# Kernel optimization log

Measured on AMD Instinct MI355X. Metric: run time of the kernel, lower is better.

The kernel has to match this reference:

```python
import jax, jax.numpy as jnp
import numpy as np

CTX = 2048
D_IN = 2048
D_OUT = 2048
N_HEADS = 16
HEAD_DIM = D_OUT // N_HEADS
ROPE_BASE = 10000.0


def rope_tables(head_dim, ctx):
    inv_freq = 1.0 / (ROPE_BASE ** (jnp.arange(0, head_dim, 2, dtype=jnp.float32) / head_dim))
    angles = jnp.arange(ctx, dtype=jnp.float32)[:, None] * inv_freq[None, :]  # [ctx, hd/2]
    angles = jnp.concatenate([angles, angles], axis=1)  # [ctx, hd]
    return jnp.sin(angles), jnp.cos(angles)


def apply_rope(x, sin, cos):
    # x: [b, h, s, d]; rotate-by-half (Raschka / Llama style)
    s = x.shape[2]
    d = x.shape[3]
    x1, x2 = x[..., : d // 2], x[..., d // 2 :]
    rotated = jnp.concatenate([-x2, x1], axis=-1)
    return x * cos[:s][None, None] + rotated * sin[:s][None, None]


def setup_inputs() -> dict:
    key = jax.random.key(0)
    kx, kq, kk, kv, ko = jax.random.split(key, 5)
    scale = 0.02
    return {
        "x": jax.random.normal(kx, (2, CTX, D_IN), dtype=jnp.float32),
        "W_query": jax.random.normal(kq, (D_IN, D_OUT), dtype=jnp.float32) * scale,
        "W_key": jax.random.normal(kk, (D_IN, D_OUT), dtype=jnp.float32) * scale,
        "W_value": jax.random.normal(kv, (D_IN, D_OUT), dtype=jnp.float32) * scale,
        "W_out": jax.random.normal(ko, (D_OUT, D_OUT), dtype=jnp.float32) * scale,
    }


def reference(x, W_query, W_key, W_value, W_out):
    bs, cl, _ = x.shape
    sin, cos = rope_tables(HEAD_DIM, CTX)

    def split_heads(t):  # [b, s, d_out] -> [b, h, s, hd]
        return t.reshape(bs, cl, N_HEADS, HEAD_DIM).transpose(0, 2, 1, 3)

    q = split_heads(x @ W_query)
    k = split_heads(x @ W_key)
    v = split_heads(x @ W_value)

    q = apply_rope(q, sin, cos)
    k = apply_rope(k, sin, cos)

    # NOTE: original module does NOT scale by 1/sqrt(head_dim)
    scores = jnp.einsum("bhqd,bhkd->bhqk", q, k)
    causal = jnp.triu(jnp.ones((cl, cl), dtype=bool), k=1)
    scores = jnp.where(causal[None, None], -jnp.inf, scores)
    weights = jax.nn.softmax(scores, axis=-1)
    ctx = jnp.einsum("bhqk,bhkd->bhqd", weights, v)
    ctx = ctx.transpose(0, 2, 1, 3).reshape(bs, cl, N_HEADS * HEAD_DIM)
    return ctx @ W_out
```

## Files before the change

### kernel.cpp

```cpp
#include <hip/hip_runtime.h>
#include <cstdint>
#include <cstddef>

typedef _Float16 f16;
typedef _Float16 f16x8 __attribute__((ext_vector_type(8)));
typedef _Float16 f16x4 __attribute__((ext_vector_type(4)));
typedef float    f32x4 __attribute__((ext_vector_type(4)));

#define S_CTX 2048
#define NH 16
#define DH 128

#define BAR() asm volatile("s_barrier" ::: "memory")
#define VMW(n) asm volatile("s_waitcnt vmcnt(" #n ")" ::: "memory")

__device__ __forceinline__ void gload16(const void* g, void* l) {
  __builtin_amdgcn_global_load_lds(
      (const __attribute__((address_space(1))) void*)g,
      (__attribute__((address_space(3))) void*)l, 16, 0, 0);
}

__global__ void prep(const float* __restrict__ x,
                     const float* __restrict__ w0, const float* __restrict__ w1,
                     const float* __restrict__ w2, const float* __restrict__ w3,
                     f16* __restrict__ xb,
                     f16* __restrict__ o0, f16* __restrict__ o1,
                     f16* __restrict__ o2, f16* __restrict__ o3,
                     float* __restrict__ sint, float* __restrict__ cost) {
  const int bid = blockIdx.x, tid = threadIdx.x;
  if (bid < 512) {
    int idx = bid * 256 + tid;
    int j = idx & 63, s = idx >> 6;
    float invf = __expf(-(float)(2 * j) * (1.0f / 128.0f) * 9.210340371976184f);
    float a = (float)s * invf;
    sint[idx] = sinf(a);
    cost[idx] = cosf(a);
  } else if (bid < 8704) {
    int i = ((bid - 512) * 256 + tid) * 4;
    float4 v = *(const float4*)(x + i);
    f16x4 o; o[0] = (f16)v.x; o[1] = (f16)v.y; o[2] = (f16)v.z; o[3] = (f16)v.w;
    *(f16x4*)(xb + i) = o;
  } else {
    int b2 = bid - 8704;
    int z = b2 >> 12, rem = b2 & 4095;
    int by = rem >> 6, bx = rem & 63;
    int tx = tid & 31, ty = tid >> 5;
    const float* in; f16* out;
    switch (z) {
      case 0: in = w0; out = o0; break;
      case 1: in = w1; out = o1; break;
      case 2: in = w2; out = o2; break;
      default: in = w3; out = o3; break;
    }
    __shared__ float tl[32][33];
    int xc = bx * 32 + tx, yc = by * 32 + ty;
#pragma unroll
    for (int r = 0; r < 32; r += 8)
      tl[ty + r][tx] = in[(size_t)(yc + r) * 2048 + xc];
    __syncthreads();
    int xo = by * 32 + tx, yo = bx * 32 + ty;
#pragma unroll
    for (int r = 0; r < 32; r += 8)
      out[(size_t)(yo + r) * 2048 + xo] = (f16)tl[tx][ty + r];
  }
}

__global__ __launch_bounds__(512, 1)
void gemm_qk(const f16* __restrict__ A, const f16* __restrict__ wqT,
             const f16* __restrict__ wkT,
             f16* __restrict__ qb, f16* __restrict__ kb,
             const float* __restrict__ sint, const float* __restrict__ cost) {
  extern __shared__ __align__(16) char lds[];
  const int tid = threadIdx.x, lane = tid & 63;
  const int wvi = tid >> 6, wm = wvi >> 2, wn = wvi & 3;
  const int gcol = blockIdx.x * 256;
  const int proj = gcol >> 11;
  const int col0 = gcol & 2047;
  const int row0 = blockIdx.y * 256;
  const f16* Bt = proj ? wkT : wqT;

  const int ca0 = tid, ca1 = tid + 512;
  const int ra0 = ca0 >> 2, ra1 = ca1 >> 2;
  const int sa0 = (ca0 & 3) ^ ((ra0 >> 1) & 3);
  const int sa1 = (ca1 & 3) ^ ((ra1 >> 1) & 3);
  const f16* gA0 = A + (size_t)(row0 + ra0) * 2048 + sa0 * 8;
  const f16* gA1 = A + (size_t)(row0 + ra1) * 2048 + sa1 * 8;
  const f16* gB0 = Bt + (size_t)(col0 + ra0) * 2048 + sa0 * 8;
  const f16* gB1 = Bt + (size_t)(col0 + ra1) * 2048 + sa1 * 8;

  const int kslot = lane >> 4;
  int aoff[8], boff[4];
#pragma unroll
  for (int i = 0; i < 8; i++) {
    int row = wm * 128 + i * 16 + (lane & 15);
    aoff[i] = row * 64 + ((kslot ^ ((row >> 1) & 3)) << 4);
  }
#pragma unroll
  for (int j = 0; j < 4; j++) {
    int rb = (wn >> 1) * 128 + (wn & 1) * 32 + (j & 1) * 16 + (j >> 1) * 64 + (lane & 15);
    boff[j] = rb * 64 + ((kslot ^ ((rb >> 1) & 3)) << 4);
  }

  f32x4 acc[8][4] = {};

#define QKPH(SLOT, HS, SSLOT, DOSTAGE, WN) do {                                \
    const char* As_ = lds + (SLOT) * 32768;                                    \
    const char* Bs_ = As_ + 16384;                                             \
    f16x8 af[8], bf[4];                                                        \
    _Pragma("unroll") for (int i_ = 0; i_ < 8; i_++)                           \
      af[i_] = *(const f16x8*)(As_ + aoff[i_]);                                \
    _Pragma("unroll") for (int j_ = 0; j_ < 4; j_++)                           \
      bf[j_] = *(const f16x8*)(Bs_ + boff[j_]);                                \
    if (DOSTAGE) {                                                             \
      char* dA = lds + (SSLOT) * 32768;                                        \
      gload16(gA0 + (HS) * 32, dA + ca0 * 16);                                 \
      gload16(gA1 + (HS) * 32, dA + ca1 * 16);                                 \
      gload16(gB0 + (HS) * 32, dA + 16384 + ca0 * 16);                         \
      gload16(gB1 + (HS) * 32, dA + 16384 + ca1 * 16);                         \
    }                                                                          \
    asm volatile("s_waitcnt vmcnt(" #WN ")" ::: "memory");                     \
    BAR();                                                                     \
    __builtin_amdgcn_s_setprio(1);                                             \
    _Pragma("unroll") for (int i_ = 0; i_ < 8; i_++)                           \
      _Pragma("unroll") for (int j_ = 0; j_ < 4; j_++)                         \
        acc[i_][j_] = __builtin_amdgcn_mfma_f32_16x16x32_f16(af[i_], bf[j_],   \
                                                             acc[i_][j_], 0, 0, 0); \
    __builtin_amdgcn_s_setprio(0);                                             \
    BAR();                                                                     \
  } while (0)

#pragma unroll
  for (int h = 0; h < 2; h++) {
    char* dA = lds + h * 32768;
    gload16(gA0 + h * 32, dA + ca0 * 16);
    gload16(gA1 + h * 32, dA + ca1 * 16);
    gload16(gB0 + h * 32, dA + 16384 + ca0 * 16);
    gload16(gB1 + h * 32, dA + 16384 + ca1 * 16);
  }
  VMW(4); BAR();

  for (int t = 0; t < 20; ++t) {
    const int hb = 3 * t;
    QKPH(0, hb + 2, 2, 1, 4);
    QKPH(1, hb + 3, 0, 1, 4);
    QKPH(2, hb + 4, 1, 1, 4);
  }
  QKPH(0, 62, 2, 1, 4);
  QKPH(1, 63, 0, 1, 4);
  QKPH(2, 0, 0, 0, 0);
  QKPH(0, 0, 0, 0, 63);
#undef QKPH

  const int b = row0 >> 11, sb = row0 & 2047;
  f16* dst = proj ? kb : qb;
  const int h = (col0 >> 7) + (wn >> 1);
#pragma unroll
  for (int i = 0; i < 8; i++)
#pragma unroll
    for (int jj = 0; jj < 2; jj++)
#pragma unroll
      for (int r = 0; r < 4; r++) {
        int s = sb + wm * 128 + i * 16 + (lane >> 4) * 4 + r;
        int d = (wn & 1) * 32 + jj * 16 + (lane & 15);
        float cv = cost[s * 64 + d], sv = sint[s * 64 + d];
        float x1 = acc[i][jj][r], x2 = acc[i][jj + 2][r];
        size_t base = ((size_t)(b * NH + h) * S_CTX + s) << 7;
        dst[base + d]      = (f16)(x1 * cv - x2 * sv);
        dst[base + d + 64] = (f16)(x2 * cv + x1 * sv);
      }
}

template<int MODE>
__global__ __launch_bounds__(512, 1)
void gemm8(const f16* __restrict__ A, const f16* __restrict__ Bt,
           f16* __restrict__ vtb, float* __restrict__ of) {
  extern __shared__ __align__(16) char lds[];
#define RING_A(e) (lds + (e) * 16384)
#define RING_B(e) (lds + 65536 + (e) * 8192)
  const int tid = threadIdx.x, lane = tid & 63;
  const int wvi = tid >> 6, wm = wvi >> 1, wn = wvi & 1;
  const int col0 = blockIdx.x * 128;
  const int row0 = blockIdx.y * 256;

  const int ca0 = tid, ca1 = tid + 512, cb0 = tid;
  const int rAs0 = ca0 >> 2, rAs1 = ca1 >> 2, rBs0 = cb0 >> 2;
  const int sA0 = (ca0 & 3) ^ ((rAs0 >> 1) & 3);
  const int sA1 = (ca1 & 3) ^ ((rAs1 >> 1) & 3);
  const int sB0 = (cb0 & 3) ^ ((rBs0 >> 1) & 3);
  const f16* gA0 = A + (size_t)(row0 + rAs0) * 2048 + sA0 * 8;
  const f16* gA1 = A + (size_t)(row0 + rAs1) * 2048 + sA1 * 8;
  const f16* gB0 = Bt + (size_t)(col0 + rBs0) * 2048 + sB0 * 8;

  const int kslot = lane >> 4;
  int aoff[4], boff[4];
#pragma unroll
  for (int i = 0; i < 4; i++) {
    int row = wm * 64 + i * 16 + (lane & 15);
    aoff[i] = row * 64 + ((kslot ^ ((row >> 1) & 3)) << 4);
  }
#pragma unroll
  for (int j = 0; j < 4; j++) {
    int rb = wn * 32 + (j & 1) * 16 + (j >> 1) * 64 + (lane & 15);
    boff[j] = rb * 64 + ((kslot ^ ((rb >> 1) & 3)) << 4);
  }

  f32x4 acc[4][4] = {};

#define PH8(SLOT, HS, DOSTAGE, WN) do {                                        \
    const char* As_ = RING_A(SLOT);                                            \
    const char* Bs_ = RING_B(SLOT);                                            \
    f16x8 af[4], bf[4];                                                        \
    _Pragma("unroll") for (int i_ = 0; i_ < 4; i_++)                           \
      af[i_] = *(const f16x8*)(As_ + aoff[i_]);                                \
    _Pragma("unroll") for (int j_ = 0; j_ < 4; j_++)                           \
      bf[j_] = *(const f16x8*)(Bs_ + boff[j_]);                                \
    if (DOSTAGE) {                                                             \
      gload16(gA0 + (HS) * 32, RING_A((HS) & 3) + ca0 * 16);                   \
      gload16(gA1 + (HS) * 32, RING_A((HS) & 3) + ca1 * 16);                   \
      gload16(gB0 + (HS) * 32, RING_B((HS) & 3) + cb0 * 16);                   \
    }                                                                          \
    asm volatile("s_waitcnt vmcnt(" #WN ")" ::: "memory");                     \
    BAR();                                                                     \
    __builtin_amdgcn_s_setprio(1);                                             \
    _Pragma("unroll") for (int i_ = 0; i_ < 4; i_++)                           \
      _Pragma("unroll") for (int j_ = 0; j_ < 4; j_++)                         \
        acc[i_][j_] = __builtin_amdgcn_mfma_f32_16x16x32_f16(af[i_], bf[j_],   \
                                                             acc[i_][j_], 0, 0, 0); \
    __builtin_amdgcn_s_setprio(0);                                             \
    BAR();                                                                     \
  } while (0)

#pragma unroll
  for (int h = 0; h < 3; h++) {
    gload16(gA0 + h * 32, RING_A(h) + ca0 * 16);
    gload16(gA1 + h * 32, RING_A(h) + ca1 * 16);
    gload16(gB0 + h * 32, RING_B(h) + cb0 * 16);
  }
  VMW(6); BAR();

  for (int t = 0; t < 15; ++t) {
    const int p = t * 4;
    PH8(0, p + 3, 1, 6);
    PH8(1, p + 4, 1, 6);
    PH8(2, p + 5, 1, 6);
    PH8(3, p + 6, 1, 6);
  }
  PH8(0, 63, 1, 6);
  PH8(1, 0, 0, 3);
  PH8(2, 0, 0, 0);
  PH8(3, 0, 0, 63);
#undef PH8

  const int b = row0 >> 11, sbase = row0 & 2047;

  if (MODE == 2) {
#pragma unroll
    for (int i = 0; i < 4; i++)
#pragma unroll
      for (int j = 0; j < 4; j++)
#pragma unroll
        for (int r = 0; r < 4; r++) {
          int row = row0 + wm * 64 + i * 16 + (lane >> 4) * 4 + r;
          int col = col0 + wn * 32 + (j & 1) * 16 + (j >> 1) * 64 + (lane & 15);
          of[(size_t)row * 2048 + col] = acc[i][j][r];
        }
  } else {
    const int h = col0 >> 7;
    f16x4* ldsv = (f16x4*)lds;
#pragma unroll
    for (int i = 0; i < 4; i++)
#pragma unroll
      for (int j = 0; j < 4; j++) {
        f16x4 v;
#pragma unroll
        for (int r = 0; r < 4; r++) v[r] = (f16)acc[i][j][r];
        int su = wm * 16 + i * 4 + (lane >> 4);
        int d  = wn * 32 + (j & 1) * 16 + (j >> 1) * 64 + (lane & 15);
        ldsv[d * 64 + (su ^ ((d << 1) & 63))] = v;
      }
    __syncthreads();
#pragma unroll
    for (int it = 0; it < 8; ++it) {
      int o = it * 512 + tid;
      int d = o >> 5, c = o & 31;
      int xc = (d << 1) & 63;
      f16x4 lo = ldsv[d * 64 + ((2 * c) ^ xc)];
      f16x4 hi = ldsv[d * 64 + ((2 * c + 1) ^ xc)];
      f16x8 vv;
      vv[0] = lo[0]; vv[1] = lo[1]; vv[2] = lo[2]; vv[3] = lo[3];
      vv[4] = hi[0]; vv[5] = hi[1]; vv[6] = hi[2]; vv[7] = hi[3];
      *(f16x8*)&vtb[((size_t)(b * NH + h) * DH + d) * S_CTX + sbase + c * 8] = vv;
    }
  }
#undef RING_A
#undef RING_B
}

__global__ __launch_bounds__(512)
void attn_k(const f16* __restrict__ q, const f16* __restrict__ kk,
            const f16* __restrict__ vt, f16* __restrict__ ctx) {
  __shared__ __align__(16) f16 Ks[2][64 * 128];
  __shared__ __align__(16) f16 Vs[2][128 * 64];
  __shared__ __align__(16) f16 Pl[8][16 * 64];
  const int tid = threadIdx.x, lane = tid & 63, wv = tid >> 6;
  const int bh = blockIdx.y;
  const int b = bh >> 4, h = bh & 15;
  const size_t plane = (size_t)bh * (S_CTX * DH);
  const f16* Qp = q + plane;
  const f16* Kp = kk + plane;
  const f16* Vp = vt + plane;
  const float LOG2E = 1.4426950408889634f;

  const int ck0 = tid, ck1 = tid + 512;
  const int cv0 = tid, cv1 = tid + 512;

  for (int half = 0; half < 2; half++) {
    const int Q = half ? (15 - (int)blockIdx.x) : (int)blockIdx.x;
    const int q0 = Q * 128;
    const int NT = 2 * Q + 2;

    f16x8 qf[4];
    {
      const f16* qq = Qp + (size_t)(q0 + wv * 16 + (lane & 15)) * DH + ((lane >> 4) * 8);
#pragma unroll
      for (int ks = 0; ks < 4; ks++) {
        qf[ks] = *(const f16x8*)(qq + ks * 32);
#pragma unroll
        for (int e = 0; e < 8; e++) qf[ks][e] = (f16)((float)qf[ks][e] * LOG2E);
      }
    }
    float m_[4], l_[4];
    f32x4 o[8] = {};
#pragma unroll
    for (int r = 0; r < 4; r++) { m_[r] = -3e38f; l_[r] = 0.f; }

    {
      int rk0 = ck0 >> 4, rk1 = ck1 >> 4;
      gload16(Kp + (size_t)rk0 * DH + (((ck0 & 15) ^ (rk0 & 7)) * 8), &Ks[0][ck0 * 8]);
      gload16(Kp + (size_t)rk1 * DH + (((ck1 & 15) ^ (rk1 & 7)) * 8), &Ks[0][ck1 * 8]);
      int rv0 = cv0 >> 3, rv1 = cv1 >> 3;
      gload16(Vp + (size_t)rv0 * S_CTX + (((cv0 & 7) ^ (rv0 & 7)) * 8), &Vs[0][cv0 * 8]);
      gload16(Vp + (size_t)rv1 * S_CTX + (((cv1 & 7) ^ (rv1 & 7)) * 8), &Vs[0][cv1 * 8]);
    }
    VMW(0); BAR();

    int cur = 0;
    for (int t = 0; t < NT; t++) {
      if (t + 1 < NT) {
        const f16* Kt = Kp + (size_t)(t + 1) * 64 * DH;
        const f16* Vt = Vp + (size_t)(t + 1) * 64;
        int nb = cur ^ 1;
        int rk0 = ck0 >> 4, rk1 = ck1 >> 4;
        gload16(Kt + (size_t)rk0 * DH + (((ck0 & 15) ^ (rk0 & 7)) * 8), &Ks[nb][ck0 * 8]);
        gload16(Kt + (size_t)rk1 * DH + (((ck1 & 15) ^ (rk1 & 7)) * 8), &Ks[nb][ck1 * 8]);
        int rv0 = cv0 >> 3, rv1 = cv1 >> 3;
        gload16(Vt + (size_t)rv0 * S_CTX + (((cv0 & 7) ^ (rv0 & 7)) * 8), &Vs[nb][cv0 * 8]);
        gload16(Vt + (size_t)rv1 * S_CTX + (((cv1 & 7) ^ (rv1 & 7)) * 8), &Vs[nb][cv1 * 8]);
      }

      const f16* Ksc = Ks[cur];
      const f16* Vsc = Vs[cur];

      f32x4 st[4] = {};
#pragma unroll
      for (int n = 0; n < 4; n++) {
        int rK = n * 16 + (lane & 15);
#pragma unroll
        for (int ks = 0; ks < 4; ks++) {
          int slot = ks * 4 + (lane >> 4);
          f16x8 kf = *(const f16x8*)&Ksc[rK * 128 + ((slot ^ (rK & 7)) << 3)];
          st[n] = __builtin_amdgcn_mfma_f32_16x16x32_f16(qf[ks], kf, st[n], 0, 0, 0);
        }
      }
      if (t >= 2 * Q) {
#pragma unroll
        for (int n = 0; n < 4; n++)
#pragma unroll
          for (int r = 0; r < 4; r++) {
            int kvc = t * 64 + n * 16 + (lane & 15);
            int qr = q0 + wv * 16 + (lane >> 4) * 4 + r;
            if (kvc > qr) st[n][r] = -3e38f;
          }
      }
      float mx[4];
#pragma unroll
      for (int r = 0; r < 4; r++)
        mx[r] = fmaxf(fmaxf(st[0][r], st[1][r]), fmaxf(st[2][r], st[3][r]));
#pragma unroll
      for (int msk = 1; msk < 16; msk <<= 1)
#pragma unroll
        for (int r = 0; r < 4; r++) mx[r] = fmaxf(mx[r], __shfl_xor(mx[r], msk));
      bool need = false;
#pragma unroll
      for (int r = 0; r < 4; r++) need = need || (mx[r] > m_[r] + 8.0f);
      if (__any(need)) {
#pragma unroll
        for (int r = 0; r < 4; r++) {
          float nm = fmaxf(m_[r], mx[r]);
          float al = __builtin_amdgcn_exp2f(m_[r] - nm);
          m_[r] = nm;
          l_[r] *= al;
#pragma unroll
          for (int j = 0; j < 8; j++) o[j][r] *= al;
        }
      }
      float ps[4] = {0.f, 0.f, 0.f, 0.f};
      float pvv[4][4];
#pragma unroll
      for (int n = 0; n < 4; n++)
#pragma unroll
        for (int r = 0; r < 4; r++) {
          float p = __builtin_amdgcn_exp2f(st[n][r] - m_[r]);
          pvv[n][r] = p; ps[r] += p;
        }
#pragma unroll
      for (int msk = 1; msk < 16; msk <<= 1)
#pragma unroll
        for (int r = 0; r < 4; r++) ps[r] += __shfl_xor(ps[r], msk);
#pragma unroll
      for (int r = 0; r < 4; r++) l_[r] += ps[r];

      f16* Pw = Pl[wv];
#pragma unroll
      for (int n = 0; n < 4; n++)
#pragma unroll
        for (int r = 0; r < 4; r++) {
          int rowp = (lane >> 4) * 4 + r;
          int colp = n * 16 + (lane & 15);
          Pw[rowp * 64 + (((colp >> 3) ^ (rowp & 7)) << 3) + (colp & 7)] = (f16)pvv[n][r];
        }
#pragma unroll
      for (int ks = 0; ks < 2; ks++) {
        int rowp = lane & 15;
        int slotp = ks * 4 + (lane >> 4);
        f16x8 pa = *(const f16x8*)&Pw[rowp * 64 + ((slotp ^ (rowp & 7)) << 3)];
#pragma unroll
        for (int j = 0; j < 8; j++) {
          int rv = j * 16 + (lane & 15);
          int slotv = ks * 4 + (lane >> 4);
          f16x8 vf = *(const f16x8*)&Vsc[rv * 64 + ((slotv ^ (rv & 7)) << 3)];
          o[j] = __builtin_amdgcn_mfma_f32_16x16x32_f16(pa, vf, o[j], 0, 0, 0);
        }
      }

      VMW(0); BAR();
      cur ^= 1;
    }

#pragma unroll
    for (int j = 0; j < 8; j++)
#pragma unroll
      for (int r = 0; r < 4; r++) {
        int qr = q0 + wv * 16 + (lane >> 4) * 4 + r;
        int dd = h * 128 + j * 16 + (lane & 15);
        ctx[((size_t)(b * S_CTX + qr) * 2048) + dd] = (f16)(o[j][r] / l_[r]);
      }
  }
}

extern "C" void kernel_launch(void* const* d_in, const int* in_sizes, int n_in,
                              void* d_out, int out_size, void* d_ws, size_t ws_size,
                              hipStream_t stream) {
  (void)in_sizes; (void)n_in; (void)out_size; (void)ws_size;
  const float* x  = (const float*)d_in[0];
  const float* Wq = (const float*)d_in[1];
  const float* Wk = (const float*)d_in[2];
  const float* Wv = (const float*)d_in[3];
  const float* Wo = (const float*)d_in[4];
  float* out = (float*)d_out;
  char* ws = (char*)d_ws;

  f16*   xb   = (f16*)(ws);
  f16*   ctxb = (f16*)(ws);
  f16*   wqT  = (f16*)(ws + 16777216);
  f16*   wkT  = (f16*)(ws + 25165824);
  f16*   wvT  = (f16*)(ws + 33554432);
  f16*   woT  = (f16*)(ws + 41943040);
  f16*   qb   = (f16*)(ws + 50331648);
  f16*   kb   = (f16*)(ws + 67108864);
  f16*   vtb  = (f16*)(ws + 83886080);
  float* sint = (float*)(ws + 100663296);
  float* cost = (float*)(ws + 101187584);

  prep<<<dim3(25088), dim3(256), 0, stream>>>(x, Wq, Wk, Wv, Wo, xb,
                                              wqT, wkT, wvT, woT, sint, cost);
  gemm_qk<<<dim3(16, 16), dim3(512), 98304, stream>>>(xb, wqT, wkT, qb, kb, sint, cost);
  gemm8<1><<<dim3(16, 16), dim3(512), 98304, stream>>>(xb, wvT, vtb, nullptr);
  attn_k<<<dim3(8, 32), dim3(512), 0, stream>>>(qb, kb, vtb, ctxb);
  gemm8<2><<<dim3(16, 16), dim3(512), 98304, stream>>>(ctxb, woT, nullptr, out);
}
```

Measured before the change: 274.9 us.

## Give each attention wave two 16-row query tiles with half the threads

```diff
diff --git a/kernel.cpp b/kernel.cpp
--- a/kernel.cpp
+++ b/kernel.cpp
@@ -13,6 +13,7 @@
 
 #define BAR() asm volatile("s_barrier" ::: "memory")
 #define VMW(n) asm volatile("s_waitcnt vmcnt(" #n ")" ::: "memory")
+#define MF(a, b, c) __builtin_amdgcn_mfma_f32_16x16x32_f16((a), (b), (c), 0, 0, 0)
 
 __device__ __forceinline__ void gload16(const void* g, void* l) {
   __builtin_amdgcn_global_load_lds(
@@ -123,8 +124,7 @@
     __builtin_amdgcn_s_setprio(1);                                             \
     _Pragma("unroll") for (int i_ = 0; i_ < 8; i_++)                           \
       _Pragma("unroll") for (int j_ = 0; j_ < 4; j_++)                         \
-        acc[i_][j_] = __builtin_amdgcn_mfma_f32_16x16x32_f16(af[i_], bf[j_],   \
-                                                             acc[i_][j_], 0, 0, 0); \
+        acc[i_][j_] = MF(af[i_], bf[j_], acc[i_][j_]);                         \
     __builtin_amdgcn_s_setprio(0);                                             \
     BAR();                                                                     \
   } while (0)
@@ -224,8 +224,7 @@
     __builtin_amdgcn_s_setprio(1);                                             \
     _Pragma("unroll") for (int i_ = 0; i_ < 4; i_++)                           \
       _Pragma("unroll") for (int j_ = 0; j_ < 4; j_++)                         \
-        acc[i_][j_] = __builtin_amdgcn_mfma_f32_16x16x32_f16(af[i_], bf[j_],   \
-                                                             acc[i_][j_], 0, 0, 0); \
+        acc[i_][j_] = MF(af[i_], bf[j_], acc[i_][j_]);                         \
     __builtin_amdgcn_s_setprio(0);                                             \
     BAR();                                                                     \
   } while (0)
@@ -296,12 +295,12 @@
 #undef RING_B
 }
 
-__global__ __launch_bounds__(512)
+__global__ __launch_bounds__(256)
 void attn_k(const f16* __restrict__ q, const f16* __restrict__ kk,
             const f16* __restrict__ vt, f16* __restrict__ ctx) {
   __shared__ __align__(16) f16 Ks[2][64 * 128];
   __shared__ __align__(16) f16 Vs[2][128 * 64];
-  __shared__ __align__(16) f16 Pl[8][16 * 64];
+  __shared__ __align__(16) f16 Pl[4][2][16 * 64];
   const int tid = threadIdx.x, lane = tid & 63, wv = tid >> 6;
   const int bh = blockIdx.y;
   const int b = bh >> 4, h = bh & 15;
@@ -311,57 +310,55 @@
   const f16* Vp = vt + plane;
   const float LOG2E = 1.4426950408889634f;
 
-  const int ck0 = tid, ck1 = tid + 512;
-  const int cv0 = tid, cv1 = tid + 512;
+#define STAGE(T, BUF) do {                                                      \
+    const f16* Kt = Kp + (size_t)(T) * 64 * DH;                                 \
+    const f16* Vt = Vp + (size_t)(T) * 64;                                      \
+    _Pragma("unroll") for (int j_ = 0; j_ < 4; j_++) {                          \
+      int c = tid + j_ * 256; int rk = c >> 4;                                  \
+      gload16(Kt + (size_t)rk * DH + (((c & 15) ^ (rk & 7)) * 8), &Ks[BUF][c * 8]); \
+    }                                                                           \
+    _Pragma("unroll") for (int j_ = 0; j_ < 4; j_++) {                          \
+      int c = tid + j_ * 256; int rv = c >> 3;                                  \
+      gload16(Vt + (size_t)rv * S_CTX + (((c & 7) ^ (rv & 7)) * 8), &Vs[BUF][c * 8]); \
+    }                                                                           \
+  } while (0)
 
   for (int half = 0; half < 2; half++) {
     const int Q = half ? (15 - (int)blockIdx.x) : (int)blockIdx.x;
     const int q0 = Q * 128;
     const int NT = 2 * Q + 2;
 
-    f16x8 qf[4];
-    {
-      const f16* qq = Qp + (size_t)(q0 + wv * 16 + (lane & 15)) * DH + ((lane >> 4) * 8);
+    f16x8 qf[2][4];
+#pragma unroll
+    for (int i = 0; i < 2; i++) {
+      const f16* qq = Qp + (size_t)(q0 + i * 64 + wv * 16 + (lane & 15)) * DH + ((lane >> 4) * 8);
 #pragma unroll
       for (int ks = 0; ks < 4; ks++) {
-        qf[ks] = *(const f16x8*)(qq + ks * 32);
-#pragma unroll
-        for (int e = 0; e < 8; e++) qf[ks][e] = (f16)((float)qf[ks][e] * LOG2E);
+        qf[i][ks] = *(const f16x8*)(qq + ks * 32);
+#pragma unroll
+        for (int e = 0; e < 8; e++) qf[i][ks][e] = (f16)((float)qf[i][ks][e] * LOG2E);
       }
     }
-    float m_[4], l_[4];
-    f32x4 o[8] = {};
-#pragma unroll
-    for (int r = 0; r < 4; r++) { m_[r] = -3e38f; l_[r] = 0.f; }
-
-    {
-      int rk0 = ck0 >> 4, rk1 = ck1 >> 4;
-      gload16(Kp + (size_t)rk0 * DH + (((ck0 & 15) ^ (rk0 & 7)) * 8), &Ks[0][ck0 * 8]);
-      gload16(Kp + (size_t)rk1 * DH + (((ck1 & 15) ^ (rk1 & 7)) * 8), &Ks[0][ck1 * 8]);
-      int rv0 = cv0 >> 3, rv1 = cv1 >> 3;
-      gload16(Vp + (size_t)rv0 * S_CTX + (((cv0 & 7) ^ (rv0 & 7)) * 8), &Vs[0][cv0 * 8]);
-      gload16(Vp + (size_t)rv1 * S_CTX + (((cv1 & 7) ^ (rv1 & 7)) * 8), &Vs[0][cv1 * 8]);
-    }
+    float m_[2][4], l_[2][4];
+    f32x4 o[2][8] = {};
+#pragma unroll
+    for (int i = 0; i < 2; i++)
+#pragma unroll
+      for (int r = 0; r < 4; r++) { m_[i][r] = -3e38f; l_[i][r] = 0.f; }
+
+    STAGE(0, 0);
     VMW(0); BAR();
 
     int cur = 0;
     for (int t = 0; t < NT; t++) {
       if (t + 1 < NT) {
-        const f16* Kt = Kp + (size_t)(t + 1) * 64 * DH;
-        const f16* Vt = Vp + (size_t)(t + 1) * 64;
         int nb = cur ^ 1;
-        int rk0 = ck0 >> 4, rk1 = ck1 >> 4;
-        gload16(Kt + (size_t)rk0 * DH + (((ck0 & 15) ^ (rk0 & 7)) * 8), &Ks[nb][ck0 * 8]);
-        gload16(Kt + (size_t)rk1 * DH + (((ck1 & 15) ^ (rk1 & 7)) * 8), &Ks[nb][ck1 * 8]);
-        int rv0 = cv0 >> 3, rv1 = cv1 >> 3;
-        gload16(Vt + (size_t)rv0 * S_CTX + (((cv0 & 7) ^ (rv0 & 7)) * 8), &Vs[nb][cv0 * 8]);
-        gload16(Vt + (size_t)rv1 * S_CTX + (((cv1 & 7) ^ (rv1 & 7)) * 8), &Vs[nb][cv1 * 8]);
-      }
-
+        STAGE(t + 1, nb);
+      }
       const f16* Ksc = Ks[cur];
       const f16* Vsc = Vs[cur];
 
-      f32x4 st[4] = {};
+      f32x4 st[2][4] = {};
 #pragma unroll
       for (int n = 0; n < 4; n++) {
         int rK = n * 16 + (lane & 15);
@@ -369,77 +366,95 @@
         for (int ks = 0; ks < 4; ks++) {
           int slot = ks * 4 + (lane >> 4);
           f16x8 kf = *(const f16x8*)&Ksc[rK * 128 + ((slot ^ (rK & 7)) << 3)];
-          st[n] = __builtin_amdgcn_mfma_f32_16x16x32_f16(qf[ks], kf, st[n], 0, 0, 0);
+          st[0][n] = MF(qf[0][ks], kf, st[0][n]);
+          st[1][n] = MF(qf[1][ks], kf, st[1][n]);
         }
       }
       if (t >= 2 * Q) {
 #pragma unroll
+        for (int i = 0; i < 2; i++)
+#pragma unroll
+          for (int n = 0; n < 4; n++)
+#pragma unroll
+            for (int r = 0; r < 4; r++) {
+              int kvc = t * 64 + n * 16 + (lane & 15);
+              int qr = q0 + i * 64 + wv * 16 + (lane >> 4) * 4 + r;
+              if (kvc > qr) st[i][n][r] = -3e38f;
+            }
+      }
+      float mx[2][4];
+#pragma unroll
+      for (int i = 0; i < 2; i++) {
+#pragma unroll
+        for (int r = 0; r < 4; r++)
+          mx[i][r] = fmaxf(fmaxf(st[i][0][r], st[i][1][r]), fmaxf(st[i][2][r], st[i][3][r]));
+#pragma unroll
+        for (int msk = 1; msk < 16; msk <<= 1)
+#pragma unroll
+          for (int r = 0; r < 4; r++) mx[i][r] = fmaxf(mx[i][r], __shfl_xor(mx[i][r], msk));
+      }
+      bool need = false;
+#pragma unroll
+      for (int i = 0; i < 2; i++)
+#pragma unroll
+        for (int r = 0; r < 4; r++) need = need || (mx[i][r] > m_[i][r] + 8.0f);
+      if (__any(need)) {
+#pragma unroll
+        for (int i = 0; i < 2; i++)
+#pragma unroll
+          for (int r = 0; r < 4; r++) {
+            float nm = fmaxf(m_[i][r], mx[i][r]);
+            float al = __builtin_amdgcn_exp2f(m_[i][r] - nm);
+            m_[i][r] = nm;
+            l_[i][r] *= al;
+#pragma unroll
+            for (int j = 0; j < 8; j++) o[i][j][r] *= al;
+          }
+      }
+      float pvv[2][4][4];
+#pragma unroll
+      for (int i = 0; i < 2; i++) {
+        float ps[4] = {0.f, 0.f, 0.f, 0.f};
+#pragma unroll
         for (int n = 0; n < 4; n++)
 #pragma unroll
           for (int r = 0; r < 4; r++) {
-            int kvc = t * 64 + n * 16 + (lane & 15);
-            int qr = q0 + wv * 16 + (lane >> 4) * 4 + r;
-            if (kvc > qr) st[n][r] = -3e38f;
+            float p = __builtin_amdgcn_exp2f(st[i][n][r] - m_[i][r]);
+            pvv[i][n][r] = p; ps[r] += p;
           }
-      }
-      float mx[4];
-#pragma unroll
-      for (int r = 0; r < 4; r++)
-        mx[r] = fmaxf(fmaxf(st[0][r], st[1][r]), fmaxf(st[2][r], st[3][r]));
-#pragma unroll
-      for (int msk = 1; msk < 16; msk <<= 1)
-#pragma unroll
-        for (int r = 0; r < 4; r++) mx[r] = fmaxf(mx[r], __shfl_xor(mx[r], msk));
-      bool need = false;
-#pragma unroll
-      for (int r = 0; r < 4; r++) need = need || (mx[r] > m_[r] + 8.0f);
-      if (__any(need)) {
-#pragma unroll
-        for (int r = 0; r < 4; r++) {
-          float nm = fmaxf(m_[r], mx[r]);
-          float al = __builtin_amdgcn_exp2f(m_[r] - nm);
-          m_[r] = nm;
-          l_[r] *= al;
-#pragma unroll
-          for (int j = 0; j < 8; j++) o[j][r] *= al;
-        }
-      }
-      float ps[4] = {0.f, 0.f, 0.f, 0.f};
-      float pvv[4][4];
-#pragma unroll
-      for (int n = 0; n < 4; n++)
-#pragma unroll
-        for (int r = 0; r < 4; r++) {
-          float p = __builtin_amdgcn_exp2f(st[n][r] - m_[r]);
-          pvv[n][r] = p; ps[r] += p;
-        }
-#pragma unroll
-      for (int msk = 1; msk < 16; msk <<= 1)
-#pragma unroll
-        for (int r = 0; r < 4; r++) ps[r] += __shfl_xor(ps[r], msk);
-#pragma unroll
-      for (int r = 0; r < 4; r++) l_[r] += ps[r];
-
-      f16* Pw = Pl[wv];
-#pragma unroll
-      for (int n = 0; n < 4; n++)
-#pragma unroll
-        for (int r = 0; r < 4; r++) {
-          int rowp = (lane >> 4) * 4 + r;
-          int colp = n * 16 + (lane & 15);
-          Pw[rowp * 64 + (((colp >> 3) ^ (rowp & 7)) << 3) + (colp & 7)] = (f16)pvv[n][r];
-        }
+#pragma unroll
+        for (int msk = 1; msk < 16; msk <<= 1)
+#pragma unroll
+          for (int r = 0; r < 4; r++) ps[r] += __shfl_xor(ps[r], msk);
+#pragma unroll
+        for (int r = 0; r < 4; r++) l_[i][r] += ps[r];
+      }
+
+#pragma unroll
+      for (int i = 0; i < 2; i++) {
+        f16* Pw = Pl[wv][i];
+#pragma unroll
+        for (int n = 0; n < 4; n++)
+#pragma unroll
+          for (int r = 0; r < 4; r++) {
+            int rowp = (lane >> 4) * 4 + r;
+            int colp = n * 16 + (lane & 15);
+            Pw[rowp * 64 + (((colp >> 3) ^ (rowp & 7)) << 3) + (colp & 7)] = (f16)pvv[i][n][r];
+          }
+      }
 #pragma unroll
       for (int ks = 0; ks < 2; ks++) {
         int rowp = lane & 15;
         int slotp = ks * 4 + (lane >> 4);
-        f16x8 pa = *(const f16x8*)&Pw[rowp * 64 + ((slotp ^ (rowp & 7)) << 3)];
+        f16x8 pa0 = *(const f16x8*)&Pl[wv][0][rowp * 64 + ((slotp ^ (rowp & 7)) << 3)];
+        f16x8 pa1 = *(const f16x8*)&Pl[wv][1][rowp * 64 + ((slotp ^ (rowp & 7)) << 3)];
 #pragma unroll
         for (int j = 0; j < 8; j++) {
           int rv = j * 16 + (lane & 15);
           int slotv = ks * 4 + (lane >> 4);
           f16x8 vf = *(const f16x8*)&Vsc[rv * 64 + ((slotv ^ (rv & 7)) << 3)];
-          o[j] = __builtin_amdgcn_mfma_f32_16x16x32_f16(pa, vf, o[j], 0, 0, 0);
+          o[0][j] = MF(pa0, vf, o[0][j]);
+          o[1][j] = MF(pa1, vf, o[1][j]);
         }
       }
 
@@ -448,14 +463,17 @@
     }
 
 #pragma unroll
-    for (int j = 0; j < 8; j++)
-#pragma unroll
-      for (int r = 0; r < 4; r++) {
-        int qr = q0 + wv * 16 + (lane >> 4) * 4 + r;
-        int dd = h * 128 + j * 16 + (lane & 15);
-        ctx[((size_t)(b * S_CTX + qr) * 2048) + dd] = (f16)(o[j][r] / l_[r]);
-      }
-  }
+    for (int i = 0; i < 2; i++)
+#pragma unroll
+      for (int j = 0; j < 8; j++)
+#pragma unroll
+        for (int r = 0; r < 4; r++) {
+          int qr = q0 + i * 64 + wv * 16 + (lane >> 4) * 4 + r;
+          int dd = h * 128 + j * 16 + (lane & 15);
+          ctx[((size_t)(b * S_CTX + qr) * 2048) + dd] = (f16)(o[i][j][r] / l_[i][r]);
+        }
+  }
+#undef STAGE
 }
 
 extern "C" void kernel_launch(void* const* d_in, const int* in_sizes, int n_in,
@@ -486,6 +504,6 @@
                                               wqT, wkT, wvT, woT, sint, cost);
   gemm_qk<<<dim3(16, 16), dim3(512), 98304, stream>>>(xb, wqT, wkT, qb, kb, sint, cost);
   gemm8<1><<<dim3(16, 16), dim3(512), 98304, stream>>>(xb, wvT, vtb, nullptr);
-  attn_k<<<dim3(8, 32), dim3(512), 0, stream>>>(qb, kb, vtb, ctxb);
+  attn_k<<<dim3(8, 32), dim3(256), 0, stream>>>(qb, kb, vtb, ctxb);
   gemm8<2><<<dim3(16, 16), dim3(512), 98304, stream>>>(ctxb, woT, nullptr, out);
 }
```

After: 316.9 us. +15.3%, slower.
